# Performance work log

Hardware: AMD Instinct MI355X
Metric: run time of the kernel (lower is better)

## Reference

```python
import jax, jax.numpy as jnp
import numpy as np

LAMBDA = 0.7
K = 3
HIDDEN = 8
IN_F = 512
OUT_F = 256
N = 4096


def _gat_layer(x, adj, W, a):
    # h = fc(x); e[i,j] = attn([h_i ; h_j]) = h_i @ a[:F] + h_j @ a[F:]
    # (same math as the N*N repeat/cat/linear, without materializing [N*N, 2F])
    h = x @ W                      # [N, F]
    F_ = h.shape[1]
    src = h @ a[:F_]               # [N, 1]
    dst = h @ a[F_:]               # [N, 1]
    e = src + dst.T                # [N, N]
    att = jax.nn.softmax(e, axis=1) * adj
    return jax.nn.elu(att @ h)     # [N, F]


def setup_inputs() -> dict:
    key = jax.random.key(0)
    ks = jax.random.split(key, 8)
    x = jax.random.normal(ks[0], (N, IN_F), dtype=jnp.float32)
    # binarized sparse-ish adjacency stored densely (avg degree ~41)
    adj = (jax.random.uniform(ks[1], (N, N)) < 0.01).astype(jnp.float32)
    W1 = jax.random.normal(ks[2], (IN_F, HIDDEN), dtype=jnp.float32) * (1.0 / np.sqrt(IN_F))
    a1 = jax.random.normal(ks[3], (2 * HIDDEN, 1), dtype=jnp.float32) * (1.0 / np.sqrt(2 * HIDDEN))
    W2 = jax.random.normal(ks[4], (HIDDEN, 1), dtype=jnp.float32) * (1.0 / np.sqrt(HIDDEN))
    a2 = jax.random.normal(ks[5], (2, 1), dtype=jnp.float32)
    W_sgc = jax.random.normal(ks[6], (IN_F * K, OUT_F), dtype=jnp.float32) * (1.0 / np.sqrt(IN_F * K))
    b_sgc = jnp.zeros((OUT_F,), dtype=jnp.float32)
    return {"x": x, "adj": adj, "W1": W1, "a1": a1, "W2": W2, "a2": a2,
            "W_sgc": W_sgc, "b_sgc": b_sgc}


def reference(x, adj, W1, a1, W2, a2, W_sgc, b_sgc):
    # GAT scoring head (dropout p=0.6 is identity at inference)
    h1 = _gat_layer(x, adj, W1, a1)
    node_scores = _gat_layer(h1, adj, W2, a2)        # [N, 1]

    # K-hop adjacency powers
    adj_list = [adj]
    for _ in range(1, K):
        adj_list.append(adj_list[-1] @ adj)

    # dynamic per-row masking (row-broadcast of node_scores > lambda)
    change_mask = (node_scores > LAMBDA).astype(adj.dtype)  # [N, 1] broadcasts over cols
    for k in range(K - 1):
        adj_list[k] = adj_list[k] * change_mask
        adj_list[k + 1] = adj_list[k + 1] * (1.0 - change_mask)

    # SGC: concat K hop-aggregated features, then linear
    agg = jnp.concatenate([A @ x for A in adj_list], axis=1)  # [N, K*IN_F]
    return agg @ W_sgc + b_sgc
```

## Files before the change

### kernel.cpp

```cpp
#include <hip/hip_runtime.h>
#include <hip/hip_bf16.h>
#include <cstddef>

#define NNODE 4096
#define INF   512
#define OUTF  256
#define HID   8
#define CAP   128

typedef __attribute__((ext_vector_type(8))) short short8;
typedef __attribute__((ext_vector_type(4))) float f32x4;

__device__ __forceinline__ unsigned short f2bf(float f){
  unsigned int u = __float_as_uint(f);
  u += 0x7fffu + ((u >> 16) & 1u);
  return (unsigned short)(u >> 16);
}
__device__ __forceinline__ float bf2f(unsigned short s){
  return __uint_as_float((unsigned int)s << 16);
}

__global__ __launch_bounds__(256) void build_csr(const float* __restrict__ adj,
                                                 int* __restrict__ deg,
                                                 int* __restrict__ cols){
  int row = blockIdx.x, tid = threadIdx.x;
  __shared__ int cnt;
  if (tid == 0) cnt = 0;
  __syncthreads();
  const float4* arow = (const float4*)(adj + (size_t)row * NNODE);
  int* crow = cols + (size_t)row * CAP;
  #pragma unroll
  for (int k = 0; k < 4; k++){
    int idx = k * 256 + tid;
    float4 v = arow[idx];
    int n0 = (v.x != 0.f), n1 = (v.y != 0.f), n2 = (v.z != 0.f), n3 = (v.w != 0.f);
    int m = n0 + n1 + n2 + n3;
    if (m){
      int base = atomicAdd(&cnt, m);
      int c = idx * 4;
      if (n0){ if (base < CAP) crow[base] = c;     base++; }
      if (n1){ if (base < CAP) crow[base] = c + 1; base++; }
      if (n2){ if (base < CAP) crow[base] = c + 2; base++; }
      if (n3){ if (base < CAP) crow[base] = c + 3; }
    }
  }
  __syncthreads();
  int c = cnt > CAP ? CAP : cnt;
  int c8 = (c + 7) & ~7;
  if (c8 > CAP) c8 = CAP;
  if (tid < c8 - c) crow[c + tid] = NNODE;
  if (tid == 0) deg[row] = c8;
}

__global__ __launch_bounds__(256) void gat_h(const float* __restrict__ x,
                                             const float* __restrict__ W1,
                                             const float* __restrict__ a1,
                                             float* __restrict__ h,
                                             float* __restrict__ dstv,
                                             unsigned short* __restrict__ xb){
  if (blockIdx.x == 0 && threadIdx.x < HID)
    h[(size_t)NNODE * HID + threadIdx.x] = 0.f;
  int wave = threadIdx.x >> 6, lane = threadIdx.x & 63;
  int row = blockIdx.x * 4 + wave;
  const float* xr = x + (size_t)row * INF;
  unsigned short* xbr = xb + (size_t)row * INF;
  float acc[HID];
  #pragma unroll
  for (int f = 0; f < HID; f++) acc[f] = 0.f;
  for (int k = lane; k < INF; k += 64){
    float xv = xr[k];
    xbr[k] = f2bf(xv);
    const float* wp = W1 + (size_t)k * HID;
    #pragma unroll
    for (int f = 0; f < HID; f++) acc[f] += xv * wp[f];
  }
  #pragma unroll
  for (int f = 0; f < HID; f++)
    for (int o = 32; o >= 1; o >>= 1) acc[f] += __shfl_xor(acc[f], o, 64);
  if (lane == 0){
    float d = 0.f;
    #pragma unroll
    for (int f = 0; f < HID; f++){ h[(size_t)row*HID + f] = acc[f]; d += acc[f] * a1[HID + f]; }
    dstv[row] = d;
  }
}

__global__ __launch_bounds__(1024) void softmax_p(const float* __restrict__ dstv,
                                                  float* __restrict__ p){
  __shared__ float red[16];
  int tid = threadIdx.x, lane = tid & 63, wv = tid >> 6;
  if (tid == 0) p[NNODE] = 0.f;
  float mx = -INFINITY;
  for (int i = tid; i < NNODE; i += 1024) mx = fmaxf(mx, dstv[i]);
  #pragma unroll
  for (int o = 32; o >= 1; o >>= 1) mx = fmaxf(mx, __shfl_xor(mx, o, 64));
  if (lane == 0) red[wv] = mx;
  __syncthreads();
  mx = red[0];
  #pragma unroll
  for (int k = 1; k < 16; k++) mx = fmaxf(mx, red[k]);
  __syncthreads();
  float sum = 0.f;
  for (int i = tid; i < NNODE; i += 1024){ float e = expf(dstv[i] - mx); p[i] = e; sum += e; }
  #pragma unroll
  for (int o = 32; o >= 1; o >>= 1) sum += __shfl_xor(sum, o, 64);
  if (lane == 0) red[wv] = sum;
  __syncthreads();
  float tot = 0.f;
  #pragma unroll
  for (int k = 0; k < 16; k++) tot += red[k];
  float inv = 1.0f / tot;
  for (int i = tid; i < NNODE; i += 1024) p[i] *= inv;
}

__global__ __launch_bounds__(256) void gat_agg1(const float* __restrict__ h,
                                                const float* __restrict__ p,
                                                const int* __restrict__ deg,
                                                const int* __restrict__ cols,
                                                const float* __restrict__ W2,
                                                float* __restrict__ h2){
  int wave = threadIdx.x >> 6, lane = threadIdx.x & 63;
  int row = blockIdx.x * 4 + wave;
  const int* cl = cols + (size_t)row * CAP;
  int d = deg[row];
  int ng = lane >> 3;
  int f  = lane & 7;
  float acc = 0.f;
  for (int n = ng; n < d; n += 8){
    int j = cl[n];
    acc += p[j] * h[(size_t)j * HID + f];
  }
  acc += __shfl_xor(acc, 8, 64);
  acc += __shfl_xor(acc, 16, 64);
  acc += __shfl_xor(acc, 32, 64);
  float e = acc > 0.f ? acc : expm1f(acc);
  float t = e * W2[f];
  t += __shfl_xor(t, 1, 64);
  t += __shfl_xor(t, 2, 64);
  t += __shfl_xor(t, 4, 64);
  if (lane == 0) h2[row] = t;
}

__global__ __launch_bounds__(1024) void softmax_q(const float* __restrict__ h2,
                                                  const float* __restrict__ a2,
                                                  float* __restrict__ q){
  __shared__ float red[16];
  int tid = threadIdx.x, lane = tid & 63, wv = tid >> 6;
  if (tid == 0) q[NNODE] = 0.f;
  float s2 = a2[1];
  float mx = -INFINITY;
  for (int i = tid; i < NNODE; i += 1024) mx = fmaxf(mx, s2 * h2[i]);
  #pragma unroll
  for (int o = 32; o >= 1; o >>= 1) mx = fmaxf(mx, __shfl_xor(mx, o, 64));
  if (lane == 0) red[wv] = mx;
  __syncthreads();
  mx = red[0];
  #pragma unroll
  for (int k = 1; k < 16; k++) mx = fmaxf(mx, red[k]);
  __syncthreads();
  float sum = 0.f;
  for (int i = tid; i < NNODE; i += 1024){ float e = expf(s2 * h2[i] - mx); q[i] = e; sum += e; }
  #pragma unroll
  for (int o = 32; o >= 1; o >>= 1) sum += __shfl_xor(sum, o, 64);
  if (lane == 0) red[wv] = sum;
  __syncthreads();
  float tot = 0.f;
  #pragma unroll
  for (int k = 0; k < 16; k++) tot += red[k];
  float inv = 1.0f / tot;
  for (int i = tid; i < NNODE; i += 1024) q[i] = q[i] * inv * h2[i];
}

__global__ __launch_bounds__(256) void scores_mask(const float* __restrict__ q,
                                                   const int* __restrict__ deg,
                                                   const int* __restrict__ cols,
                                                   float* __restrict__ maskf){
  int wave = threadIdx.x >> 6, lane = threadIdx.x & 63;
  int row = blockIdx.x * 4 + wave;
  const int* cl = cols + (size_t)row * CAP;
  int d = deg[row];
  float s = 0.f;
  for (int n = lane; n < d; n += 64) s += q[cl[n]];
  #pragma unroll
  for (int o = 32; o >= 1; o >>= 1) s += __shfl_xor(s, o, 64);
  if (lane == 0){
    float e = s > 0.f ? s : expm1f(s);
    maskf[row] = (e > 0.7f) ? 1.0f : 0.0f;
  }
}

__global__ void convert_w(const float* __restrict__ Wsgc, unsigned short* __restrict__ wbT,
                          unsigned short* __restrict__ Gb,
                          unsigned short* __restrict__ T1,
                          unsigned short* __restrict__ T2){
  int idx = blockIdx.x * 256 + threadIdx.x;
  if (idx < 512) Gb[(size_t)NNODE * 512 + idx] = 0;
  if (idx < 256){ T1[(size_t)NNODE * 256 + idx] = 0; T2[(size_t)NNODE * 256 + idx] = 0; }
  if (idx >= 512 * 512) return;
  int c = idx >> 9, k = idx & 511;
  float val = (c < 256) ? Wsgc[(size_t)k * OUTF + c]
                        : Wsgc[(size_t)(1024 + k) * OUTF + (c - 256)];
  wbT[idx] = f2bf(val);
}

__global__ __launch_bounds__(256) void gemm_xw(const unsigned short* __restrict__ XB,
                                               const unsigned short* __restrict__ BT,
                                               unsigned short* __restrict__ Gb){
  __shared__ unsigned short As[128][72];
  __shared__ unsigned short Bs[128][72];
  int tid = threadIdx.x;
  int wave = tid >> 6, lane = tid & 63;
  int row0 = blockIdx.x * 128;
  int col0 = blockIdx.y * 128;
  int wr = wave >> 1, wc = wave & 1;
  f32x4 acc[4][4];
  #pragma unroll
  for (int i = 0; i < 4; i++)
    #pragma unroll
    for (int j = 0; j < 4; j++)
      #pragma unroll
      for (int e = 0; e < 4; e++) acc[i][j][e] = 0.f;

  int mrow = lane & 15;
  int kq = (lane >> 4) * 8;

  for (int k0 = 0; k0 < 512; k0 += 64){
    #pragma unroll
    for (int ps = 0; ps < 4; ps++){
      int idx = ps * 256 + tid;
      int r = idx >> 3;
      int ko = (idx & 7) * 8;
      *(int4*)(&As[r][ko]) = *(const int4*)(XB + ((size_t)(row0 + r) * 512 + k0 + ko));
      *(int4*)(&Bs[r][ko]) = *(const int4*)(BT + ((size_t)(col0 + r) * 512 + k0 + ko));
    }
    __syncthreads();
    #pragma unroll
    for (int kk = 0; kk < 2; kk++){
      short8 a[4], b[4];
      #pragma unroll
      for (int i = 0; i < 4; i++)
        a[i] = *(const short8*)(&As[wr * 64 + i * 16 + mrow][kk * 32 + kq]);
      #pragma unroll
      for (int j = 0; j < 4; j++)
        b[j] = *(const short8*)(&Bs[wc * 64 + j * 16 + mrow][kk * 32 + kq]);
      #pragma unroll
      for (int i = 0; i < 4; i++)
        #pragma unroll
        for (int j = 0; j < 4; j++)
          acc[i][j] = __builtin_amdgcn_mfma_f32_16x16x32_bf16(a[i], b[j], acc[i][j], 0, 0, 0);
    }
    __syncthreads();
  }
  int crow = (lane >> 4) * 4;
  int ccol = lane & 15;
  #pragma unroll
  for (int i = 0; i < 4; i++)
    #pragma unroll
    for (int j = 0; j < 4; j++)
      #pragma unroll
      for (int e = 0; e < 4; e++){
        int r = row0 + wr * 64 + i * 16 + crow + e;
        int c = col0 + wc * 64 + j * 16 + ccol;
        Gb[(size_t)r * 512 + c] = f2bf(acc[i][j][e]);
      }
}

__global__ __launch_bounds__(256) void hop_bf(const unsigned short* __restrict__ in, int instride,
                                              int colbase,
                                              unsigned short* __restrict__ out,
                                              const int* __restrict__ deg,
                                              const int* __restrict__ cols){
  int wave = threadIdx.x >> 6, lane = threadIdx.x & 63;
  int row = blockIdx.x * 4 + wave;
  const int* cl = cols + (size_t)row * CAP;
  int d = deg[row];
  int half = lane >> 5, cid = lane & 31;
  const unsigned short* src = in + colbase + cid * 8;
  float acc[8];
  #pragma unroll
  for (int e = 0; e < 8; e++) acc[e] = 0.f;
  int n = 0;
  for (; n + 16 <= d; n += 16){
    int j0 = cl[n +      half], j1 = cl[n + 2  + half], j2 = cl[n + 4  + half], j3 = cl[n + 6  + half];
    int j4 = cl[n + 8  + half], j5 = cl[n + 10 + half], j6 = cl[n + 12 + half], j7 = cl[n + 14 + half];
    short8 v0 = *(const short8*)(src + (size_t)j0 * instride);
    short8 v1 = *(const short8*)(src + (size_t)j1 * instride);
    short8 v2 = *(const short8*)(src + (size_t)j2 * instride);
    short8 v3 = *(const short8*)(src + (size_t)j3 * instride);
    short8 v4 = *(const short8*)(src + (size_t)j4 * instride);
    short8 v5 = *(const short8*)(src + (size_t)j5 * instride);
    short8 v6 = *(const short8*)(src + (size_t)j6 * instride);
    short8 v7 = *(const short8*)(src + (size_t)j7 * instride);
    #pragma unroll
    for (int e = 0; e < 8; e++){
      acc[e] += bf2f((unsigned short)v0[e]) + bf2f((unsigned short)v1[e])
              + bf2f((unsigned short)v2[e]) + bf2f((unsigned short)v3[e])
              + bf2f((unsigned short)v4[e]) + bf2f((unsigned short)v5[e])
              + bf2f((unsigned short)v6[e]) + bf2f((unsigned short)v7[e]);
    }
  }
  if (n < d){
    int j0 = cl[n + half], j1 = cl[n + 2 + half], j2 = cl[n + 4 + half], j3 = cl[n + 6 + half];
    short8 v0 = *(const short8*)(src + (size_t)j0 * instride);
    short8 v1 = *(const short8*)(src + (size_t)j1 * instride);
    short8 v2 = *(const short8*)(src + (size_t)j2 * instride);
    short8 v3 = *(const short8*)(src + (size_t)j3 * instride);
    #pragma unroll
    for (int e = 0; e < 8; e++){
      acc[e] += bf2f((unsigned short)v0[e]) + bf2f((unsigned short)v1[e])
              + bf2f((unsigned short)v2[e]) + bf2f((unsigned short)v3[e]);
    }
  }
  #pragma unroll
  for (int e = 0; e < 8; e++) acc[e] += __shfl_xor(acc[e], 32, 64);
  if (half == 0){
    union { short8 v; unsigned short u[8]; } pk;
    #pragma unroll
    for (int e = 0; e < 8; e++) pk.u[e] = f2bf(acc[e]);
    *(short8*)(out + (size_t)row * OUTF + cid * 8) = pk.v;
  }
}

__global__ __launch_bounds__(256) void hop_final_bf(const unsigned short* __restrict__ Gb,
                                                    const unsigned short* __restrict__ T2,
                                                    const float* __restrict__ maskf,
                                                    const float* __restrict__ b,
                                                    float* __restrict__ out,
                                                    const int* __restrict__ deg,
                                                    const int* __restrict__ cols){
  int wave = threadIdx.x >> 6, lane = threadIdx.x & 63;
  int row = blockIdx.x * 4 + wave;
  const int* cl = cols + (size_t)row * CAP;
  int d = deg[row];
  bool m = maskf[row] != 0.0f;
  const unsigned short* base = m ? Gb : T2;
  int instride = m ? 512 : 256;
  int half = lane >> 5, cid = lane & 31;
  const unsigned short* src = base + cid * 8;
  float acc[8];
  #pragma unroll
  for (int e = 0; e < 8; e++) acc[e] = 0.f;
  int n = 0;
  for (; n + 16 <= d; n += 16){
    int j0 = cl[n +      half], j1 = cl[n + 2  + half], j2 = cl[n + 4  + half], j3 = cl[n + 6  + half];
    int j4 = cl[n + 8  + half], j5 = cl[n + 10 + half], j6 = cl[n + 12 + half], j7 = cl[n + 14 + half];
    short8 v0 = *(const short8*)(src + (size_t)j0 * instride);
    short8 v1 = *(const short8*)(src + (size_t)j1 * instride);
    short8 v2 = *(const short8*)(src + (size_t)j2 * instride);
    short8 v3 = *(const short8*)(src + (size_t)j3 * instride);
    short8 v4 = *(const short8*)(src + (size_t)j4 * instride);
    short8 v5 = *(const short8*)(src + (size_t)j5 * instride);
    short8 v6 = *(const short8*)(src + (size_t)j6 * instride);
    short8 v7 = *(const short8*)(src + (size_t)j7 * instride);
    #pragma unroll
    for (int e = 0; e < 8; e++){
      acc[e] += bf2f((unsigned short)v0[e]) + bf2f((unsigned short)v1[e])
              + bf2f((unsigned short)v2[e]) + bf2f((unsigned short)v3[e])
              + bf2f((unsigned short)v4[e]) + bf2f((unsigned short)v5[e])
              + bf2f((unsigned short)v6[e]) + bf2f((unsigned short)v7[e]);
    }
  }
  if (n < d){
    int j0 = cl[n + half], j1 = cl[n + 2 + half], j2 = cl[n + 4 + half], j3 = cl[n + 6 + half];
    short8 v0 = *(const short8*)(src + (size_t)j0 * instride);
    short8 v1 = *(const short8*)(src + (size_t)j1 * instride);
    short8 v2 = *(const short8*)(src + (size_t)j2 * instride);
    short8 v3 = *(const short8*)(src + (size_t)j3 * instride);
    #pragma unroll
    for (int e = 0; e < 8; e++){
      acc[e] += bf2f((unsigned short)v0[e]) + bf2f((unsigned short)v1[e])
              + bf2f((unsigned short)v2[e]) + bf2f((unsigned short)v3[e]);
    }
  }
  #pragma unroll
  for (int e = 0; e < 8; e++) acc[e] += __shfl_xor(acc[e], 32, 64);
  if (half == 0){
    f32x4 b0 = ((const f32x4*)(b + cid * 8))[0];
    f32x4 b1 = ((const f32x4*)(b + cid * 8 + 4))[0];
    f32x4 o0, o1;
    #pragma unroll
    for (int e = 0; e < 4; e++){ o0[e] = acc[e] + b0[e]; o1[e] = acc[4 + e] + b1[e]; }
    float* orow = out + (size_t)row * OUTF + cid * 8;
    ((f32x4*)orow)[0] = o0;
    ((f32x4*)(orow + 4))[0] = o1;
  }
}

extern "C" void kernel_launch(void* const* d_in, const int* in_sizes, int n_in,
                              void* d_out, int out_size, void* d_ws, size_t ws_size,
                              hipStream_t stream) {
  const float* x    = (const float*)d_in[0];
  const float* adj  = (const float*)d_in[1];
  const float* W1   = (const float*)d_in[2];
  const float* a1   = (const float*)d_in[3];
  const float* W2   = (const float*)d_in[4];
  const float* a2   = (const float*)d_in[5];
  const float* Wsgc = (const float*)d_in[6];
  const float* bsgc = (const float*)d_in[7];
  float* out = (float*)d_out;

  char* w = (char*)d_ws;
  size_t off = 0;
  auto carve = [&](size_t bytes) -> char* {
    char* p = w + off;
    off += (bytes + 255) & ~(size_t)255;
    return p;
  };
  int*   deg   = (int*)carve((size_t)NNODE * 4);
  int*   cols  = (int*)carve((size_t)NNODE * CAP * 4);
  float* h     = (float*)carve((size_t)(NNODE + 1) * HID * 4);
  float* dstv  = (float*)carve((size_t)NNODE * 4);
  float* p     = (float*)carve((size_t)(NNODE + 1) * 4);
  float* h2    = (float*)carve((size_t)NNODE * 4);
  float* q     = (float*)carve((size_t)(NNODE + 1) * 4);
  float* maskf = (float*)carve((size_t)NNODE * 4);
  unsigned short* wbT = (unsigned short*)carve((size_t)512 * 512 * 2);
  unsigned short* xb  = (unsigned short*)carve((size_t)NNODE * INF * 2);
  unsigned short* Gb  = (unsigned short*)carve((size_t)(NNODE + 1) * 512 * 2);
  unsigned short* T1  = (unsigned short*)carve((size_t)(NNODE + 1) * OUTF * 2);
  unsigned short* T2  = (unsigned short*)carve((size_t)(NNODE + 1) * OUTF * 2);

  build_csr<<<NNODE, 256, 0, stream>>>(adj, deg, cols);

  gat_h<<<NNODE / 4, 256, 0, stream>>>(x, W1, a1, h, dstv, xb);
  softmax_p<<<1, 1024, 0, stream>>>(dstv, p);
  gat_agg1<<<NNODE / 4, 256, 0, stream>>>(h, p, deg, cols, W2, h2);
  softmax_q<<<1, 1024, 0, stream>>>(h2, a2, q);
  scores_mask<<<NNODE / 4, 256, 0, stream>>>(q, deg, cols, maskf);

  convert_w<<<1024, 256, 0, stream>>>(Wsgc, wbT, Gb, T1, T2);
  dim3 gg(32, 4);
  gemm_xw<<<gg, 256, 0, stream>>>(xb, wbT, Gb);

  hop_bf<<<NNODE / 4, 256, 0, stream>>>(Gb, 512, 256, T1, deg, cols);
  hop_bf<<<NNODE / 4, 256, 0, stream>>>(T1, 256, 0,  T2, deg, cols);
  hop_final_bf<<<NNODE / 4, 256, 0, stream>>>(Gb, T2, maskf, bsgc, out, deg, cols);
}
```

Baseline: 172.6 us.

## Merge independent stages into multi-role kernels and redundantly compute softmax per block

Cuts the launch sequence from eleven kernels to five by merging independent work into shared launches that branch on block index. CSR build, the GAT projection and the weight conversion now run as one kernel. The GEMM runs beside the first GAT aggregation, and the first hop runs beside score masking. The single-block global softmax kernels are gone: every aggregation block recomputes the full 4096-element softmax into shared memory. This removes serial single-block launches and launch gaps, at the cost of redundant reductions and larger shared-memory use that may reduce occupancy.

```diff
diff --git a/kernel.cpp b/kernel.cpp
--- a/kernel.cpp
+++ b/kernel.cpp
@@ -20,249 +20,295 @@
   return __uint_as_float((unsigned int)s << 16);
 }
 
-__global__ __launch_bounds__(256) void build_csr(const float* __restrict__ adj,
-                                                 int* __restrict__ deg,
-                                                 int* __restrict__ cols){
-  int row = blockIdx.x, tid = threadIdx.x;
-  __shared__ int cnt;
-  if (tid == 0) cnt = 0;
-  __syncthreads();
-  const float4* arow = (const float4*)(adj + (size_t)row * NNODE);
-  int* crow = cols + (size_t)row * CAP;
-  #pragma unroll
-  for (int k = 0; k < 4; k++){
-    int idx = k * 256 + tid;
-    float4 v = arow[idx];
-    int n0 = (v.x != 0.f), n1 = (v.y != 0.f), n2 = (v.z != 0.f), n3 = (v.w != 0.f);
-    int m = n0 + n1 + n2 + n3;
-    if (m){
-      int base = atomicAdd(&cnt, m);
-      int c = idx * 4;
-      if (n0){ if (base < CAP) crow[base] = c;     base++; }
-      if (n1){ if (base < CAP) crow[base] = c + 1; base++; }
-      if (n2){ if (base < CAP) crow[base] = c + 2; base++; }
-      if (n3){ if (base < CAP) crow[base] = c + 3; }
-    }
-  }
-  __syncthreads();
-  int c = cnt > CAP ? CAP : cnt;
-  int c8 = (c + 7) & ~7;
-  if (c8 > CAP) c8 = CAP;
-  if (tid < c8 - c) crow[c + tid] = NNODE;
-  if (tid == 0) deg[row] = c8;
-}
-
-__global__ __launch_bounds__(256) void gat_h(const float* __restrict__ x,
+__global__ __launch_bounds__(256) void front(const float* __restrict__ adj,
+                                             int* __restrict__ deg,
+                                             int* __restrict__ cols,
+                                             const float* __restrict__ x,
                                              const float* __restrict__ W1,
                                              const float* __restrict__ a1,
                                              float* __restrict__ h,
                                              float* __restrict__ dstv,
-                                             unsigned short* __restrict__ xb){
-  if (blockIdx.x == 0 && threadIdx.x < HID)
-    h[(size_t)NNODE * HID + threadIdx.x] = 0.f;
-  int wave = threadIdx.x >> 6, lane = threadIdx.x & 63;
-  int row = blockIdx.x * 4 + wave;
-  const float* xr = x + (size_t)row * INF;
-  unsigned short* xbr = xb + (size_t)row * INF;
-  float acc[HID];
-  #pragma unroll
-  for (int f = 0; f < HID; f++) acc[f] = 0.f;
-  for (int k = lane; k < INF; k += 64){
-    float xv = xr[k];
-    xbr[k] = f2bf(xv);
-    const float* wp = W1 + (size_t)k * HID;
-    #pragma unroll
-    for (int f = 0; f < HID; f++) acc[f] += xv * wp[f];
-  }
-  #pragma unroll
-  for (int f = 0; f < HID; f++)
-    for (int o = 32; o >= 1; o >>= 1) acc[f] += __shfl_xor(acc[f], o, 64);
-  if (lane == 0){
-    float d = 0.f;
-    #pragma unroll
-    for (int f = 0; f < HID; f++){ h[(size_t)row*HID + f] = acc[f]; d += acc[f] * a1[HID + f]; }
-    dstv[row] = d;
-  }
-}
-
-__global__ __launch_bounds__(1024) void softmax_p(const float* __restrict__ dstv,
-                                                  float* __restrict__ p){
-  __shared__ float red[16];
-  int tid = threadIdx.x, lane = tid & 63, wv = tid >> 6;
-  if (tid == 0) p[NNODE] = 0.f;
-  float mx = -INFINITY;
-  for (int i = tid; i < NNODE; i += 1024) mx = fmaxf(mx, dstv[i]);
-  #pragma unroll
-  for (int o = 32; o >= 1; o >>= 1) mx = fmaxf(mx, __shfl_xor(mx, o, 64));
-  if (lane == 0) red[wv] = mx;
-  __syncthreads();
-  mx = red[0];
-  #pragma unroll
-  for (int k = 1; k < 16; k++) mx = fmaxf(mx, red[k]);
-  __syncthreads();
-  float sum = 0.f;
-  for (int i = tid; i < NNODE; i += 1024){ float e = expf(dstv[i] - mx); p[i] = e; sum += e; }
-  #pragma unroll
-  for (int o = 32; o >= 1; o >>= 1) sum += __shfl_xor(sum, o, 64);
-  if (lane == 0) red[wv] = sum;
-  __syncthreads();
-  float tot = 0.f;
-  #pragma unroll
-  for (int k = 0; k < 16; k++) tot += red[k];
-  float inv = 1.0f / tot;
-  for (int i = tid; i < NNODE; i += 1024) p[i] *= inv;
-}
-
-__global__ __launch_bounds__(256) void gat_agg1(const float* __restrict__ h,
-                                                const float* __restrict__ p,
-                                                const int* __restrict__ deg,
-                                                const int* __restrict__ cols,
-                                                const float* __restrict__ W2,
-                                                float* __restrict__ h2){
-  int wave = threadIdx.x >> 6, lane = threadIdx.x & 63;
-  int row = blockIdx.x * 4 + wave;
-  const int* cl = cols + (size_t)row * CAP;
-  int d = deg[row];
-  int ng = lane >> 3;
-  int f  = lane & 7;
-  float acc = 0.f;
-  for (int n = ng; n < d; n += 8){
-    int j = cl[n];
-    acc += p[j] * h[(size_t)j * HID + f];
-  }
-  acc += __shfl_xor(acc, 8, 64);
-  acc += __shfl_xor(acc, 16, 64);
-  acc += __shfl_xor(acc, 32, 64);
-  float e = acc > 0.f ? acc : expm1f(acc);
-  float t = e * W2[f];
-  t += __shfl_xor(t, 1, 64);
-  t += __shfl_xor(t, 2, 64);
-  t += __shfl_xor(t, 4, 64);
-  if (lane == 0) h2[row] = t;
-}
-
-__global__ __launch_bounds__(1024) void softmax_q(const float* __restrict__ h2,
-                                                  const float* __restrict__ a2,
-                                                  float* __restrict__ q){
-  __shared__ float red[16];
-  int tid = threadIdx.x, lane = tid & 63, wv = tid >> 6;
-  if (tid == 0) q[NNODE] = 0.f;
-  float s2 = a2[1];
-  float mx = -INFINITY;
-  for (int i = tid; i < NNODE; i += 1024) mx = fmaxf(mx, s2 * h2[i]);
-  #pragma unroll
-  for (int o = 32; o >= 1; o >>= 1) mx = fmaxf(mx, __shfl_xor(mx, o, 64));
-  if (lane == 0) red[wv] = mx;
-  __syncthreads();
-  mx = red[0];
-  #pragma unroll
-  for (int k = 1; k < 16; k++) mx = fmaxf(mx, red[k]);
-  __syncthreads();
-  float sum = 0.f;
-  for (int i = tid; i < NNODE; i += 1024){ float e = expf(s2 * h2[i] - mx); q[i] = e; sum += e; }
-  #pragma unroll
-  for (int o = 32; o >= 1; o >>= 1) sum += __shfl_xor(sum, o, 64);
-  if (lane == 0) red[wv] = sum;
-  __syncthreads();
-  float tot = 0.f;
-  #pragma unroll
-  for (int k = 0; k < 16; k++) tot += red[k];
-  float inv = 1.0f / tot;
-  for (int i = tid; i < NNODE; i += 1024) q[i] = q[i] * inv * h2[i];
-}
-
-__global__ __launch_bounds__(256) void scores_mask(const float* __restrict__ q,
-                                                   const int* __restrict__ deg,
-                                                   const int* __restrict__ cols,
-                                                   float* __restrict__ maskf){
-  int wave = threadIdx.x >> 6, lane = threadIdx.x & 63;
-  int row = blockIdx.x * 4 + wave;
-  const int* cl = cols + (size_t)row * CAP;
-  int d = deg[row];
-  float s = 0.f;
-  for (int n = lane; n < d; n += 64) s += q[cl[n]];
-  #pragma unroll
-  for (int o = 32; o >= 1; o >>= 1) s += __shfl_xor(s, o, 64);
-  if (lane == 0){
-    float e = s > 0.f ? s : expm1f(s);
-    maskf[row] = (e > 0.7f) ? 1.0f : 0.0f;
-  }
-}
-
-__global__ void convert_w(const float* __restrict__ Wsgc, unsigned short* __restrict__ wbT,
-                          unsigned short* __restrict__ Gb,
-                          unsigned short* __restrict__ T1,
-                          unsigned short* __restrict__ T2){
-  int idx = blockIdx.x * 256 + threadIdx.x;
-  if (idx < 512) Gb[(size_t)NNODE * 512 + idx] = 0;
-  if (idx < 256){ T1[(size_t)NNODE * 256 + idx] = 0; T2[(size_t)NNODE * 256 + idx] = 0; }
-  if (idx >= 512 * 512) return;
-  int c = idx >> 9, k = idx & 511;
-  float val = (c < 256) ? Wsgc[(size_t)k * OUTF + c]
-                        : Wsgc[(size_t)(1024 + k) * OUTF + (c - 256)];
-  wbT[idx] = f2bf(val);
-}
-
-__global__ __launch_bounds__(256) void gemm_xw(const unsigned short* __restrict__ XB,
-                                               const unsigned short* __restrict__ BT,
-                                               unsigned short* __restrict__ Gb){
-  __shared__ unsigned short As[128][72];
-  __shared__ unsigned short Bs[128][72];
-  int tid = threadIdx.x;
+                                             unsigned short* __restrict__ xb,
+                                             const float* __restrict__ Wsgc,
+                                             unsigned short* __restrict__ wbT,
+                                             unsigned short* __restrict__ Gb,
+                                             unsigned short* __restrict__ T1,
+                                             unsigned short* __restrict__ T2){
+  __shared__ int cnt;
+  int bid = blockIdx.x, tid = threadIdx.x;
+
+  if (bid < NNODE){
+    int row = bid;
+    if (tid == 0) cnt = 0;
+    __syncthreads();
+    const float4* arow = (const float4*)(adj + (size_t)row * NNODE);
+    int* crow = cols + (size_t)row * CAP;
+    #pragma unroll
+    for (int k = 0; k < 4; k++){
+      int idx = k * 256 + tid;
+      float4 v = arow[idx];
+      int n0 = (v.x != 0.f), n1 = (v.y != 0.f), n2 = (v.z != 0.f), n3 = (v.w != 0.f);
+      int m = n0 + n1 + n2 + n3;
+      if (m){
+        int base = atomicAdd(&cnt, m);
+        int c = idx * 4;
+        if (n0){ if (base < CAP) crow[base] = c;     base++; }
+        if (n1){ if (base < CAP) crow[base] = c + 1; base++; }
+        if (n2){ if (base < CAP) crow[base] = c + 2; base++; }
+        if (n3){ if (base < CAP) crow[base] = c + 3; }
+      }
+    }
+    __syncthreads();
+    int c = cnt > CAP ? CAP : cnt;
+    int c8 = (c + 7) & ~7;
+    if (c8 > CAP) c8 = CAP;
+    if (tid < c8 - c) crow[c + tid] = NNODE;
+    if (tid == 0) deg[row] = c8;
+
+  } else if (bid < NNODE + 1024){
+    int b2 = bid - NNODE;
+    if (b2 == 0 && tid < HID) h[(size_t)NNODE * HID + tid] = 0.f;
+    int wave = tid >> 6, lane = tid & 63;
+    int row = b2 * 4 + wave;
+    const float* xr = x + (size_t)row * INF;
+    unsigned short* xbr = xb + (size_t)row * INF;
+    float acc[HID];
+    #pragma unroll
+    for (int f = 0; f < HID; f++) acc[f] = 0.f;
+    for (int k = lane; k < INF; k += 64){
+      float xv = xr[k];
+      xbr[k] = f2bf(xv);
+      const float* wp = W1 + (size_t)k * HID;
+      #pragma unroll
+      for (int f = 0; f < HID; f++) acc[f] += xv * wp[f];
+    }
+    #pragma unroll
+    for (int f = 0; f < HID; f++)
+      for (int o = 32; o >= 1; o >>= 1) acc[f] += __shfl_xor(acc[f], o, 64);
+    if (lane == 0){
+      float d = 0.f;
+      #pragma unroll
+      for (int f = 0; f < HID; f++){ h[(size_t)row*HID + f] = acc[f]; d += acc[f] * a1[HID + f]; }
+      dstv[row] = d;
+    }
+
+  } else {
+    int idx = (bid - NNODE - 1024) * 256 + tid;
+    if (idx < 512) Gb[(size_t)NNODE * 512 + idx] = 0;
+    if (idx < 256){ T1[(size_t)NNODE * 256 + idx] = 0; T2[(size_t)NNODE * 256 + idx] = 0; }
+    int c = idx >> 9, k = idx & 511;
+    float val = (c < 256) ? Wsgc[(size_t)k * OUTF + c]
+                          : Wsgc[(size_t)(1024 + k) * OUTF + (c - 256)];
+    wbT[idx] = f2bf(val);
+  }
+}
+
+__global__ __launch_bounds__(256) void mid(const unsigned short* __restrict__ XB,
+                                           const unsigned short* __restrict__ BT,
+                                           unsigned short* __restrict__ Gb,
+                                           const float* __restrict__ h,
+                                           const float* __restrict__ dstv,
+                                           const int* __restrict__ deg,
+                                           const int* __restrict__ cols,
+                                           const float* __restrict__ W2,
+                                           float* __restrict__ h2){
+  __shared__ union {
+    struct { unsigned short As[128][72]; unsigned short Bs[128][72]; } g;
+    struct { float p[NNODE + 1]; float red[4]; } a;
+  } sm;
+  int bid = blockIdx.x, tid = threadIdx.x;
   int wave = tid >> 6, lane = tid & 63;
-  int row0 = blockIdx.x * 128;
-  int col0 = blockIdx.y * 128;
-  int wr = wave >> 1, wc = wave & 1;
-  f32x4 acc[4][4];
-  #pragma unroll
-  for (int i = 0; i < 4; i++)
-    #pragma unroll
-    for (int j = 0; j < 4; j++)
-      #pragma unroll
-      for (int e = 0; e < 4; e++) acc[i][j][e] = 0.f;
-
-  int mrow = lane & 15;
-  int kq = (lane >> 4) * 8;
-
-  for (int k0 = 0; k0 < 512; k0 += 64){
-    #pragma unroll
-    for (int ps = 0; ps < 4; ps++){
-      int idx = ps * 256 + tid;
-      int r = idx >> 3;
-      int ko = (idx & 7) * 8;
-      *(int4*)(&As[r][ko]) = *(const int4*)(XB + ((size_t)(row0 + r) * 512 + k0 + ko));
-      *(int4*)(&Bs[r][ko]) = *(const int4*)(BT + ((size_t)(col0 + r) * 512 + k0 + ko));
-    }
-    __syncthreads();
-    #pragma unroll
-    for (int kk = 0; kk < 2; kk++){
-      short8 a[4], b[4];
-      #pragma unroll
-      for (int i = 0; i < 4; i++)
-        a[i] = *(const short8*)(&As[wr * 64 + i * 16 + mrow][kk * 32 + kq]);
+
+  if (bid < 128){
+    int bx = bid & 31, by = bid >> 5;
+    int row0 = bx * 128, col0 = by * 128;
+    int wr = wave >> 1, wc = wave & 1;
+    f32x4 acc[4][4];
+    #pragma unroll
+    for (int i = 0; i < 4; i++)
       #pragma unroll
       for (int j = 0; j < 4; j++)
-        b[j] = *(const short8*)(&Bs[wc * 64 + j * 16 + mrow][kk * 32 + kq]);
-      #pragma unroll
-      for (int i = 0; i < 4; i++)
+        #pragma unroll
+        for (int e = 0; e < 4; e++) acc[i][j][e] = 0.f;
+    int mrow = lane & 15;
+    int kq = (lane >> 4) * 8;
+    for (int k0 = 0; k0 < 512; k0 += 64){
+      #pragma unroll
+      for (int ps = 0; ps < 4; ps++){
+        int idx = ps * 256 + tid;
+        int r = idx >> 3;
+        int ko = (idx & 7) * 8;
+        *(int4*)(&sm.g.As[r][ko]) = *(const int4*)(XB + ((size_t)(row0 + r) * 512 + k0 + ko));
+        *(int4*)(&sm.g.Bs[r][ko]) = *(const int4*)(BT + ((size_t)(col0 + r) * 512 + k0 + ko));
+      }
+      __syncthreads();
+      #pragma unroll
+      for (int kk = 0; kk < 2; kk++){
+        short8 a[4], b[4];
+        #pragma unroll
+        for (int i = 0; i < 4; i++)
+          a[i] = *(const short8*)(&sm.g.As[wr * 64 + i * 16 + mrow][kk * 32 + kq]);
         #pragma unroll
         for (int j = 0; j < 4; j++)
-          acc[i][j] = __builtin_amdgcn_mfma_f32_16x16x32_bf16(a[i], b[j], acc[i][j], 0, 0, 0);
-    }
-    __syncthreads();
-  }
-  int crow = (lane >> 4) * 4;
-  int ccol = lane & 15;
-  #pragma unroll
-  for (int i = 0; i < 4; i++)
-    #pragma unroll
-    for (int j = 0; j < 4; j++)
-      #pragma unroll
-      for (int e = 0; e < 4; e++){
-        int r = row0 + wr * 64 + i * 16 + crow + e;
-        int c = col0 + wc * 64 + j * 16 + ccol;
-        Gb[(size_t)r * 512 + c] = f2bf(acc[i][j][e]);
+          b[j] = *(const short8*)(&sm.g.Bs[wc * 64 + j * 16 + mrow][kk * 32 + kq]);
+        #pragma unroll
+        for (int i = 0; i < 4; i++)
+          #pragma unroll
+          for (int j = 0; j < 4; j++)
+            acc[i][j] = __builtin_amdgcn_mfma_f32_16x16x32_bf16(a[i], b[j], acc[i][j], 0, 0, 0);
       }
+      __syncthreads();
+    }
+    int crow = (lane >> 4) * 4;
+    int ccol = lane & 15;
+    #pragma unroll
+    for (int i = 0; i < 4; i++)
+      #pragma unroll
+      for (int j = 0; j < 4; j++)
+        #pragma unroll
+        for (int e = 0; e < 4; e++){
+          int r = row0 + wr * 64 + i * 16 + crow + e;
+          int c = col0 + wc * 64 + j * 16 + ccol;
+          Gb[(size_t)r * 512 + c] = f2bf(acc[i][j][e]);
+        }
+
+  } else {
+    if (tid == 0) sm.a.p[NNODE] = 0.f;
+    float mx = -INFINITY;
+    for (int i = tid; i < NNODE; i += 256) mx = fmaxf(mx, dstv[i]);
+    #pragma unroll
+    for (int o = 32; o >= 1; o >>= 1) mx = fmaxf(mx, __shfl_xor(mx, o, 64));
+    if (lane == 0) sm.a.red[wave] = mx;
+    __syncthreads();
+    mx = fmaxf(fmaxf(sm.a.red[0], sm.a.red[1]), fmaxf(sm.a.red[2], sm.a.red[3]));
+    __syncthreads();
+    float sum = 0.f;
+    for (int i = tid; i < NNODE; i += 256){ float e = expf(dstv[i] - mx); sm.a.p[i] = e; sum += e; }
+    #pragma unroll
+    for (int o = 32; o >= 1; o >>= 1) sum += __shfl_xor(sum, o, 64);
+    if (lane == 0) sm.a.red[wave] = sum;
+    __syncthreads();
+    float inv = 1.0f / (sm.a.red[0] + sm.a.red[1] + sm.a.red[2] + sm.a.red[3]);
+    for (int i = tid; i < NNODE; i += 256) sm.a.p[i] *= inv;
+    __syncthreads();
+
+    int row = (bid - 128) * 4 + wave;
+    const int* cl = cols + (size_t)row * CAP;
+    int d = deg[row];
+    int ng = lane >> 3;
+    int f  = lane & 7;
+    float acc = 0.f;
+    for (int n = ng; n < d; n += 8){
+      int j = cl[n];
+      acc += sm.a.p[j] * h[(size_t)j * HID + f];
+    }
+    acc += __shfl_xor(acc, 8, 64);
+    acc += __shfl_xor(acc, 16, 64);
+    acc += __shfl_xor(acc, 32, 64);
+    float e = acc > 0.f ? acc : expm1f(acc);
+    float t = e * W2[f];
+    t += __shfl_xor(t, 1, 64);
+    t += __shfl_xor(t, 2, 64);
+    t += __shfl_xor(t, 4, 64);
+    if (lane == 0) h2[row] = t;
+  }
+}
+
+__global__ __launch_bounds__(256) void sc_hop1(const unsigned short* __restrict__ Gb,
+                                               unsigned short* __restrict__ T1,
+                                               const float* __restrict__ h2,
+                                               const float* __restrict__ a2,
+                                               const int* __restrict__ deg,
+                                               const int* __restrict__ cols,
+                                               float* __restrict__ maskf){
+  __shared__ float q[NNODE + 1];
+  __shared__ float red[4];
+  int bid = blockIdx.x, tid = threadIdx.x;
+  int wave = tid >> 6, lane = tid & 63;
+
+  if (bid < 1024){
+    int row = bid * 4 + wave;
+    const int* cl = cols + (size_t)row * CAP;
+    int d = deg[row];
+    int half = lane >> 5, cid = lane & 31;
+    const unsigned short* src = Gb + 256 + cid * 8;
+    float acc[8];
+    #pragma unroll
+    for (int e = 0; e < 8; e++) acc[e] = 0.f;
+    int n = 0;
+    for (; n + 16 <= d; n += 16){
+      int j0 = cl[n +      half], j1 = cl[n + 2  + half], j2 = cl[n + 4  + half], j3 = cl[n + 6  + half];
+      int j4 = cl[n + 8  + half], j5 = cl[n + 10 + half], j6 = cl[n + 12 + half], j7 = cl[n + 14 + half];
+      short8 v0 = *(const short8*)(src + (size_t)j0 * 512);
+      short8 v1 = *(const short8*)(src + (size_t)j1 * 512);
+      short8 v2 = *(const short8*)(src + (size_t)j2 * 512);
+      short8 v3 = *(const short8*)(src + (size_t)j3 * 512);
+      short8 v4 = *(const short8*)(src + (size_t)j4 * 512);
+      short8 v5 = *(const short8*)(src + (size_t)j5 * 512);
+      short8 v6 = *(const short8*)(src + (size_t)j6 * 512);
+      short8 v7 = *(const short8*)(src + (size_t)j7 * 512);
+      #pragma unroll
+      for (int e = 0; e < 8; e++){
+        acc[e] += bf2f((unsigned short)v0[e]) + bf2f((unsigned short)v1[e])
+                + bf2f((unsigned short)v2[e]) + bf2f((unsigned short)v3[e])
+                + bf2f((unsigned short)v4[e]) + bf2f((unsigned short)v5[e])
+                + bf2f((unsigned short)v6[e]) + bf2f((unsigned short)v7[e]);
+      }
+    }
+    if (n < d){
+      int j0 = cl[n + half], j1 = cl[n + 2 + half], j2 = cl[n + 4 + half], j3 = cl[n + 6 + half];
+      short8 v0 = *(const short8*)(src + (size_t)j0 * 512);
+      short8 v1 = *(const short8*)(src + (size_t)j1 * 512);
+      short8 v2 = *(const short8*)(src + (size_t)j2 * 512);
+      short8 v3 = *(const short8*)(src + (size_t)j3 * 512);
+      #pragma unroll
+      for (int e = 0; e < 8; e++){
+        acc[e] += bf2f((unsigned short)v0[e]) + bf2f((unsigned short)v1[e])
+                + bf2f((unsigned short)v2[e]) + bf2f((unsigned short)v3[e]);
+      }
+    }
+    #pragma unroll
+    for (int e = 0; e < 8; e++) acc[e] += __shfl_xor(acc[e], 32, 64);
+    if (half == 0){
+      union { short8 v; unsigned short u[8]; } pk;
+      #pragma unroll
+      for (int e = 0; e < 8; e++) pk.u[e] = f2bf(acc[e]);
+      *(short8*)(T1 + (size_t)row * OUTF + cid * 8) = pk.v;
+    }
+
+  } else {
+    float s2 = a2[1];
+    if (tid == 0) q[NNODE] = 0.f;
+    float mx = -INFINITY;
+    for (int i = tid; i < NNODE; i += 256) mx = fmaxf(mx, s2 * h2[i]);
+    #pragma unroll
+    for (int o = 32; o >= 1; o >>= 1) mx = fmaxf(mx, __shfl_xor(mx, o, 64));
+    if (lane == 0) red[wave] = mx;
+    __syncthreads();
+    mx = fmaxf(fmaxf(red[0], red[1]), fmaxf(red[2], red[3]));
+    __syncthreads();
+    float sum = 0.f;
+    for (int i = tid; i < NNODE; i += 256){ float e = expf(s2 * h2[i] - mx); q[i] = e; sum += e; }
+    #pragma unroll
+    for (int o = 32; o >= 1; o >>= 1) sum += __shfl_xor(sum, o, 64);
+    if (lane == 0) red[wave] = sum;
+    __syncthreads();
+    float inv = 1.0f / (red[0] + red[1] + red[2] + red[3]);
+    for (int i = tid; i < NNODE; i += 256) q[i] = q[i] * inv * h2[i];
+    __syncthreads();
+
+    int row = (bid - 1024) * 4 + wave;
+    const int* cl = cols + (size_t)row * CAP;
+    int d = deg[row];
+    float s = 0.f;
+    for (int n = lane; n < d; n += 64) s += q[cl[n]];
+    #pragma unroll
+    for (int o = 32; o >= 1; o >>= 1) s += __shfl_xor(s, o, 64);
+    if (lane == 0){
+      float e = s > 0.f ? s : expm1f(s);
+      maskf[row] = (e > 0.7f) ? 1.0f : 0.0f;
+    }
+  }
 }
 
 __global__ __launch_bounds__(256) void hop_bf(const unsigned short* __restrict__ in, int instride,
@@ -410,9 +456,7 @@
   int*   cols  = (int*)carve((size_t)NNODE * CAP * 4);
   float* h     = (float*)carve((size_t)(NNODE + 1) * HID * 4);
   float* dstv  = (float*)carve((size_t)NNODE * 4);
-  float* p     = (float*)carve((size_t)(NNODE + 1) * 4);
   float* h2    = (float*)carve((size_t)NNODE * 4);
-  float* q     = (float*)carve((size_t)(NNODE + 1) * 4);
   float* maskf = (float*)carve((size_t)NNODE * 4);
   unsigned short* wbT = (unsigned short*)carve((size_t)512 * 512 * 2);
   unsigned short* xb  = (unsigned short*)carve((size_t)NNODE * INF * 2);
@@ -420,19 +464,11 @@
   unsigned short* T1  = (unsigned short*)carve((size_t)(NNODE + 1) * OUTF * 2);
   unsigned short* T2  = (unsigned short*)carve((size_t)(NNODE + 1) * OUTF * 2);
 
-  build_csr<<<NNODE, 256, 0, stream>>>(adj, deg, cols);
-
-  gat_h<<<NNODE / 4, 256, 0, stream>>>(x, W1, a1, h, dstv, xb);
-  softmax_p<<<1, 1024, 0, stream>>>(dstv, p);
-  gat_agg1<<<NNODE / 4, 256, 0, stream>>>(h, p, deg, cols, W2, h2);
-  softmax_q<<<1, 1024, 0, stream>>>(h2, a2, q);
-  scores_mask<<<NNODE / 4, 256, 0, stream>>>(q, deg, cols, maskf);
-
-  convert_w<<<1024, 256, 0, stream>>>(Wsgc, wbT, Gb, T1, T2);
-  dim3 gg(32, 4);
-  gemm_xw<<<gg, 256, 0, stream>>>(xb, wbT, Gb);
-
-  hop_bf<<<NNODE / 4, 256, 0, stream>>>(Gb, 512, 256, T1, deg, cols);
-  hop_bf<<<NNODE / 4, 256, 0, stream>>>(T1, 256, 0,  T2, deg, cols);
+  front<<<NNODE + 1024 + 1024, 256, 0, stream>>>(adj, deg, cols,
+                                                 x, W1, a1, h, dstv, xb,
+                                                 Wsgc, wbT, Gb, T1, T2);
+  mid<<<128 + 1024, 256, 0, stream>>>(xb, wbT, Gb, h, dstv, deg, cols, W2, h2);
+  sc_hop1<<<2048, 256, 0, stream>>>(Gb, T1, h2, a2, deg, cols, maskf);
+  hop_bf<<<NNODE / 4, 256, 0, stream>>>(T1, 256, 0, T2, deg, cols);
   hop_final_bf<<<NNODE / 4, 256, 0, stream>>>(Gb, T2, maskf, bsgc, out, deg, cols);
 }
```

Result: no change. 170.2 us (-1.4%).
